# Optimization experiments

Measured on AMD Instinct MI355X. Metric: run time of the kernel, lower is better.

The kernel has to match this reference:

```python
import jax, jax.numpy as jnp
import numpy as np

B = 16384
C = 8192
NUM_TAIL = 16  # last 16 classes are target (tail) classes


def setup_inputs() -> dict:
    key = jax.random.key(0)
    k1, k2, k3 = jax.random.split(key, 3)
    inputs = jax.random.normal(k1, (B, C), dtype=jnp.float32)
    true_labels = jax.random.randint(k2, (B,), 0, C, dtype=jnp.int64)
    prev_counts = jax.random.randint(k3, (C,), 0, 64, dtype=jnp.int32)
    tail_mask = jnp.arange(C) >= (C - NUM_TAIL)  # bool [C], True for target_class_index
    return {"inputs": inputs, "true_labels": true_labels,
            "prev_counts": prev_counts, "tail_mask": tail_mask}


def reference(inputs, true_labels, prev_counts, tail_mask):
    x = jnp.nan_to_num(inputs)  # [B, C]
    num_classes = x.shape[1]

    # epoch prediction counts for the current batch (no_grad in original)
    preds = jnp.argmax(x, axis=-1)                                    # [B]
    curr_counts = jnp.zeros((num_classes,), jnp.float32).at[preds].add(1.0)  # [C]

    # differentiable softmax probabilities of the true class
    logp = jax.nn.log_softmax(x, axis=1)                              # [B, C]
    probs = jnp.exp(logp)
    p_true = jnp.take_along_axis(probs, true_labels[:, None], axis=1)[:, 0]  # [B]

    # adaptive per-sample weights (computed under no_grad in original)
    is_tail = tail_mask[true_labels]                                   # [B] bool
    prev = prev_counts[true_labels].astype(jnp.float32)                # [B]
    curr = curr_counts[true_labels]                                    # [B]
    tail_w = jnp.where((prev > 0) & (curr < prev), 4.0,
             jnp.where((prev > 0) & (curr > prev), 2.0, 3.0))
    sample_w = jnp.where(is_tail, tail_w, 1.0)                         # [B]
    sample_w = jax.lax.stop_gradient(sample_w)

    focal_w = jax.lax.stop_gradient(1.0 - p_true)                      # detached
    penalty = -jnp.log(p_true + 1e-7) * focal_w * sample_w             # [B]
    return penalty.mean() * 0.1
```

## Files before the change

### kernel.cpp

```cpp
#include <hip/hip_runtime.h>
#include <math.h>

#define BATCH 16384
#define NCLS  8192
#define NTAIL 16


__global__ void init_kernel(float* __restrict__ out, int* __restrict__ counts) {
    int t = threadIdx.x;
    if (t < NTAIL) counts[t] = 0;
    if (t == 0)    out[0] = 0.0f;
}

__global__ __launch_bounds__(256) void row_kernel(const float* __restrict__ x,
                                                  const int* __restrict__ labels,
                                                  float* __restrict__ p_true,
                                                  int* __restrict__ counts) {
    const int row = blockIdx.x;
    const int t   = threadIdx.x;
    const float4* rowp = (const float4*)(x + (size_t)row * NCLS);

    float m = -INFINITY, s = 0.0f;
    int   idx = 0;
    #pragma unroll
    for (int k = 0; k < NCLS / (256 * 4); ++k) {
        float4 v = rowp[t + k * 256];
        const int c0 = (t + k * 256) * 4;
        float e[4] = {v.x, v.y, v.z, v.w};
        #pragma unroll
        for (int j = 0; j < 4; ++j) {
            float xv = e[j];
            xv = (xv == xv) ? xv : 0.0f;
            if (xv > m) {
                s = s * __expf(m - xv) + 1.0f;
                m = xv; idx = c0 + j;
            } else {
                s += __expf(xv - m);
            }
        }
    }

    #pragma unroll
    for (int off = 32; off; off >>= 1) {
        float m2 = __shfl_down(m, off);
        float s2 = __shfl_down(s, off);
        int   i2 = __shfl_down(idx, off);
        if (m2 > m)       { s = s * __expf(m - m2) + s2; m = m2; idx = i2; }
        else if (m2 == m) { s += s2; idx = min(idx, i2); }
        else              { s += s2 * __expf(m2 - m); }
    }

    __shared__ float sm[4], ss[4];
    __shared__ int   si[4];
    const int wave = t >> 6;
    if ((t & 63) == 0) { sm[wave] = m; ss[wave] = s; si[wave] = idx; }
    __syncthreads();

    if (t == 0) {
        for (int wgi = 1; wgi < 4; ++wgi) {
            float m2 = sm[wgi], s2 = ss[wgi]; int i2 = si[wgi];
            if (m2 > m)       { s = s * __expf(m - m2) + s2; m = m2; idx = i2; }
            else if (m2 == m) { s += s2; idx = min(idx, i2); }
            else              { s += s2 * __expf(m2 - m); }
        }
        const int lab = labels[row];
        float xt = x[(size_t)row * NCLS + lab];
        xt = (xt == xt) ? xt : 0.0f;
        p_true[row] = __expf(xt - m) / s;
        if (idx >= NCLS - NTAIL) atomicAdd(&counts[idx - (NCLS - NTAIL)], 1);
    }
}

__global__ __launch_bounds__(256) void penalty_kernel(const float* __restrict__ p_true,
                                                      const int* __restrict__ labels,
                                                      const int* __restrict__ prev_counts,
                                                      const int* __restrict__ counts,
                                                      float* __restrict__ out) {
    const int i = blockIdx.x * 256 + threadIdx.x;
    const float p = p_true[i];
    const int lab = labels[i];
    float w = 1.0f;
    if (lab >= NCLS - NTAIL) {
        const int prev = prev_counts[lab];
        const int curr = counts[lab - (NCLS - NTAIL)];
        w = (prev > 0 && curr < prev) ? 4.0f
          : (prev > 0 && curr > prev) ? 2.0f
          : 3.0f;
    }
    float pen = -logf(p + 1e-7f) * (1.0f - p) * w;

    #pragma unroll
    for (int off = 32; off; off >>= 1) pen += __shfl_down(pen, off);

    __shared__ float acc[4];
    if ((threadIdx.x & 63) == 0) acc[threadIdx.x >> 6] = pen;
    __syncthreads();
    if (threadIdx.x == 0) {
        const float bs = acc[0] + acc[1] + acc[2] + acc[3];
        atomicAdd(out, bs * (0.1f / (float)BATCH));
    }
}

extern "C" void kernel_launch(void* const* d_in, const int* in_sizes, int n_in,
                              void* d_out, int out_size, void* d_ws, size_t ws_size,
                              hipStream_t stream) {
    const float* x           = (const float*)d_in[0];
    const int*   labels      = (const int*)  d_in[1];
    const int*   prev_counts = (const int*)  d_in[2];

    float* out    = (float*)d_out;
    float* p_true = (float*)d_ws;
    int*   counts = (int*)((char*)d_ws + BATCH * sizeof(float));

    init_kernel<<<1, 64, 0, stream>>>(out, counts);
    row_kernel<<<BATCH, 256, 0, stream>>>(x, labels, p_true, counts);
    penalty_kernel<<<BATCH / 256, 256, 0, stream>>>(p_true, labels, prev_counts, counts, out);
}
```

Baseline: 673.9 us.

## Split online softmax into register-held max pass then exp-sum pass

The row kernel now loads the whole row slice into registers (8 float4 per thread) first. It computes the block-wide max and argmax with four independent branch-free chains and xor shuffles, then computes the exp sum against the global max in a second pass over the registers. This removes the serial data-dependent rescaling of the online softmax and the extra exp calls in the reductions. The cost is a second block barrier and higher register pressure. The kernel is memory bound, so the gain depends on whether the compute chain was limiting overlap.

```diff
diff --git a/kernel.cpp b/kernel.cpp
--- a/kernel.cpp
+++ b/kernel.cpp
@@ -20,54 +20,73 @@
     const int t   = threadIdx.x;
     const float4* rowp = (const float4*)(x + (size_t)row * NCLS);
 
-    float m = -INFINITY, s = 0.0f;
-    int   idx = 0;
+    float4 v[8];
     #pragma unroll
-    for (int k = 0; k < NCLS / (256 * 4); ++k) {
-        float4 v = rowp[t + k * 256];
+    for (int k = 0; k < 8; ++k) {
+        float4 r = rowp[t + k * 256];
+        r.x = (r.x == r.x) ? r.x : 0.0f;
+        r.y = (r.y == r.y) ? r.y : 0.0f;
+        r.z = (r.z == r.z) ? r.z : 0.0f;
+        r.w = (r.w == r.w) ? r.w : 0.0f;
+        v[k] = r;
+    }
+
+    float mc0 = -INFINITY, mc1 = -INFINITY, mc2 = -INFINITY, mc3 = -INFINITY;
+    int   ic0 = 0, ic1 = 0, ic2 = 0, ic3 = 0;
+    #pragma unroll
+    for (int k = 0; k < 8; ++k) {
         const int c0 = (t + k * 256) * 4;
-        float e[4] = {v.x, v.y, v.z, v.w};
-        #pragma unroll
-        for (int j = 0; j < 4; ++j) {
-            float xv = e[j];
-            xv = (xv == xv) ? xv : 0.0f;
-            if (xv > m) {
-                s = s * __expf(m - xv) + 1.0f;
-                m = xv; idx = c0 + j;
-            } else {
-                s += __expf(xv - m);
-            }
-        }
+        if (v[k].x > mc0) { mc0 = v[k].x; ic0 = c0;     }
+        if (v[k].y > mc1) { mc1 = v[k].y; ic1 = c0 + 1; }
+        if (v[k].z > mc2) { mc2 = v[k].z; ic2 = c0 + 2; }
+        if (v[k].w > mc3) { mc3 = v[k].w; ic3 = c0 + 3; }
     }
+    float m = mc0; int idx = ic0;
+    if (mc1 > m || (mc1 == m && ic1 < idx)) { m = mc1; idx = ic1; }
+    if (mc2 > m || (mc2 == m && ic2 < idx)) { m = mc2; idx = ic2; }
+    if (mc3 > m || (mc3 == m && ic3 < idx)) { m = mc3; idx = ic3; }
 
     #pragma unroll
     for (int off = 32; off; off >>= 1) {
-        float m2 = __shfl_down(m, off);
-        float s2 = __shfl_down(s, off);
-        int   i2 = __shfl_down(idx, off);
-        if (m2 > m)       { s = s * __expf(m - m2) + s2; m = m2; idx = i2; }
-        else if (m2 == m) { s += s2; idx = min(idx, i2); }
-        else              { s += s2 * __expf(m2 - m); }
+        float m2 = __shfl_xor(m, off);
+        int   i2 = __shfl_xor(idx, off);
+        if (m2 > m || (m2 == m && i2 < idx)) { m = m2; idx = i2; }
     }
 
-    __shared__ float sm[4], ss[4];
+    __shared__ float sm[4];
     __shared__ int   si[4];
+    __shared__ float ssum[4];
     const int wave = t >> 6;
-    if ((t & 63) == 0) { sm[wave] = m; ss[wave] = s; si[wave] = idx; }
+    if ((t & 63) == 0) { sm[wave] = m; si[wave] = idx; }
+    __syncthreads();
+
+    float M = sm[0]; int I = si[0];
+    #pragma unroll
+    for (int w = 1; w < 4; ++w) {
+        if (sm[w] > M || (sm[w] == M && si[w] < I)) { M = sm[w]; I = si[w]; }
+    }
+
+    float s0 = 0.0f, s1 = 0.0f, s2 = 0.0f, s3 = 0.0f;
+    #pragma unroll
+    for (int k = 0; k < 8; ++k) {
+        s0 += __expf(v[k].x - M);
+        s1 += __expf(v[k].y - M);
+        s2 += __expf(v[k].z - M);
+        s3 += __expf(v[k].w - M);
+    }
+    float s = (s0 + s1) + (s2 + s3);
+    #pragma unroll
+    for (int off = 32; off; off >>= 1) s += __shfl_xor(s, off);
+    if ((t & 63) == 0) ssum[wave] = s;
     __syncthreads();
 
     if (t == 0) {
-        for (int wgi = 1; wgi < 4; ++wgi) {
-            float m2 = sm[wgi], s2 = ss[wgi]; int i2 = si[wgi];
-            if (m2 > m)       { s = s * __expf(m - m2) + s2; m = m2; idx = i2; }
-            else if (m2 == m) { s += s2; idx = min(idx, i2); }
-            else              { s += s2 * __expf(m2 - m); }
-        }
+        s = ssum[0] + ssum[1] + ssum[2] + ssum[3];
         const int lab = labels[row];
         float xt = x[(size_t)row * NCLS + lab];
         xt = (xt == xt) ? xt : 0.0f;
-        p_true[row] = __expf(xt - m) / s;
-        if (idx >= NCLS - NTAIL) atomicAdd(&counts[idx - (NCLS - NTAIL)], 1);
+        p_true[row] = __expf(xt - M) / s;
+        if (I >= NCLS - NTAIL) atomicAdd(&counts[I - (NCLS - NTAIL)], 1);
     }
 }
 
```

Result: no change. 676.2 us (+0.3%).
